# Optimization experiments

Measured on AMD Instinct MI355X. Metric: run time of the kernel, lower is better.

## Reference

```python
import jax, jax.numpy as jnp
import numpy as np

LN_EPS = 1e-5


def setup_inputs() -> dict:
    key = jax.random.key(0)
    ks = jax.random.split(key, 8)
    B, C, H, W = 16, 768, 64, 64
    cond_dim = 1024
    inp = {}
    inp["spatial_features"] = jax.random.normal(ks[0], (B, C, H, W), dtype=jnp.float32)
    inp["conditioning"] = jax.random.normal(ks[1], (B, cond_dim), dtype=jnp.float32)
    # conditioning_proj: Linear(cond_dim -> C)
    inp["w_cond"] = jax.random.normal(ks[2], (C, cond_dim), dtype=jnp.float32) * 0.02
    inp["b_cond"] = jnp.zeros((C,), dtype=jnp.float32)
    # MultiheadAttention packed in-projection [3C, C] and bias [3C]
    inp["in_proj_w"] = jax.random.normal(ks[3], (3 * C, C), dtype=jnp.float32) * 0.02
    inp["in_proj_b"] = jnp.zeros((3 * C,), dtype=jnp.float32)
    # MHA out_proj
    inp["attn_out_w"] = jax.random.normal(ks[4], (C, C), dtype=jnp.float32) * 0.02
    inp["attn_out_b"] = jnp.zeros((C,), dtype=jnp.float32)
    # output_proj Linear (dropout is identity at inference)
    inp["w_out"] = jax.random.normal(ks[5], (C, C), dtype=jnp.float32) * 0.02
    inp["b_out"] = jnp.zeros((C,), dtype=jnp.float32)
    # LayerNorm affine
    inp["ln_gamma"] = jnp.ones((C,), dtype=jnp.float32)
    inp["ln_beta"] = jnp.zeros((C,), dtype=jnp.float32)
    return inp


def reference(spatial_features, conditioning, w_cond, b_cond, in_proj_w, in_proj_b,
              attn_out_w, attn_out_b, w_out, b_out, ln_gamma, ln_beta):
    B, C, H, W = spatial_features.shape
    S = H * W
    # [B, C, H, W] -> [B, S, C]
    spatial_flat = spatial_features.reshape(B, C, S).transpose(0, 2, 1)
    # conditioning projection -> single KV token per batch: [B, C]
    cond = conditioning @ w_cond.T + b_cond
    # With a single key, softmax over the key axis is identically 1, so the
    # attention output is exactly the value vector broadcast over all queries;
    # Q and K projections have zero effect on output (and zero gradient).
    wv = in_proj_w[2 * C:]          # value rows of packed in-projection
    bv = in_proj_b[2 * C:]
    v = cond @ wv.T + bv            # [B, C]
    attn = v @ attn_out_w.T + attn_out_b  # MHA out_proj, [B, C]
    # output_proj (dropout = identity in eval)
    proj = attn @ w_out.T + b_out   # [B, C]
    # residual + LayerNorm over channel dim
    x = spatial_flat + proj[:, None, :]  # [B, S, C]
    mu = jnp.mean(x, axis=-1, keepdims=True)
    var = jnp.mean(jnp.square(x - mu), axis=-1, keepdims=True)
    y = (x - mu) * jax.lax.rsqrt(var + LN_EPS) * ln_gamma + ln_beta
    # [B, S, C] -> [B, C, H, W]
    return y.transpose(0, 2, 1).reshape(B, C, H, W)
```

## Files before the change

### kernel.cpp

```cpp
#include <hip/hip_runtime.h>

#define CDIM 768
#define SDIM 4096

typedef float nfloat4 __attribute__((ext_vector_type(4)));

__global__ __launch_bounds__(256) void small_gemm_kernel(
    const float* __restrict__ X, const float* __restrict__ W,
    const float* __restrict__ bias, float* __restrict__ out,
    int Cn, int K)
{
    int gid  = blockIdx.x * blockDim.x + threadIdx.x;
    int wid  = gid >> 6;
    int lane = threadIdx.x & 63;
    int total = 16 * Cn;
    if (wid >= total) return;
    int b = wid / Cn;
    int c = wid - b * Cn;
    const float* x = X + (size_t)b * K;
    const float* w = W + (size_t)c * K;
    float acc = 0.f;
    for (int k = lane * 4; k < K; k += 256) {
        float4 xv = *(const float4*)(x + k);
        float4 wv = *(const float4*)(w + k);
        acc += xv.x * wv.x + xv.y * wv.y + xv.z * wv.z + xv.w * wv.w;
    }
#pragma unroll
    for (int m = 32; m; m >>= 1) acc += __shfl_xor(acc, m, 64);
    if (lane == 0) out[wid] = acc + bias[c];
}

__global__ __launch_bounds__(256) void ln_stats(
    const float* __restrict__ sp, const float* __restrict__ proj,
    float* __restrict__ Aout, float* __restrict__ Bout)
{
    __shared__ float s_proj[CDIM];
    __shared__ float2 redA[4][64];
    __shared__ float2 redB[4][64];
    const int b  = blockIdx.y;
    const int s0 = blockIdx.x * 128;
    const int t  = threadIdx.x;
    for (int i = t; i < CDIM; i += 256) s_proj[i] = proj[b * CDIM + i];
    __syncthreads();

    const int lane = t & 63;
    const int wave = t >> 6;
    const float2* base = (const float2*)(sp + (size_t)b * CDIM * SDIM + s0) + lane;

    float2 A = make_float2(0.f, 0.f), B = make_float2(0.f, 0.f);
    const int cbeg = wave * (CDIM / 4);
    for (int c = cbeg; c < cbeg + CDIM / 4; c += 8) {
        float2 v[8];
#pragma unroll
        for (int k = 0; k < 8; ++k) v[k] = base[(size_t)(c + k) * (SDIM / 2)];
#pragma unroll
        for (int k = 0; k < 8; ++k) {
            float p  = s_proj[c + k];
            float ax = v[k].x + p, ay = v[k].y + p;
            A.x += ax;      A.y += ay;
            B.x += ax * ax; B.y += ay * ay;
        }
    }
    redA[wave][lane] = A;
    redB[wave][lane] = B;
    __syncthreads();

    if (t < 64) {
        float2 a = redA[0][t], bb = redB[0][t];
#pragma unroll
        for (int w = 1; w < 4; ++w) {
            a.x  += redA[w][t].x;  a.y  += redA[w][t].y;
            bb.x += redB[w][t].x;  bb.y += redB[w][t].y;
        }
        ((float2*)(Aout + (size_t)b * SDIM + s0))[t] = a;
        ((float2*)(Bout + (size_t)b * SDIM + s0))[t] = bb;
    }
}

__global__ __launch_bounds__(256) void ln_norm(
    const float* __restrict__ sp, const float* __restrict__ proj,
    const float* __restrict__ Ain, const float* __restrict__ Bin,
    const float* __restrict__ gamma, const float* __restrict__ beta,
    float* __restrict__ out)
{
    __shared__ float s_p[CDIM / 4], s_g[CDIM / 4], s_b[CDIM / 4];
    const int b      = blockIdx.y;
    const int s0     = blockIdx.x * 256;
    const int c_base = blockIdx.z * (CDIM / 4);
    const int t      = threadIdx.x;
    if (t < CDIM / 4) {
        s_p[t] = proj[b * CDIM + c_base + t];
        s_g[t] = gamma[c_base + t];
        s_b[t] = beta[c_base + t];
    }
    __syncthreads();

    const int lane = t & 63;
    const int wave = t >> 6;

    float4 A  = ((const float4*)(Ain + (size_t)b * SDIM + s0))[lane];
    float4 Bv = ((const float4*)(Bin + (size_t)b * SDIM + s0))[lane];
    const float inv = 1.f / CDIM;
    float4 mu, rs;
    mu.x = A.x * inv; mu.y = A.y * inv; mu.z = A.z * inv; mu.w = A.w * inv;
    rs.x = rsqrtf(Bv.x * inv - mu.x * mu.x + 1e-5f);
    rs.y = rsqrtf(Bv.y * inv - mu.y * mu.y + 1e-5f);
    rs.z = rsqrtf(Bv.z * inv - mu.z * mu.z + 1e-5f);
    rs.w = rsqrtf(Bv.w * inv - mu.w * mu.w + 1e-5f);

    const float4* spv  = (const float4*)(sp  + (size_t)b * CDIM * SDIM + s0) + lane;
    nfloat4*      outv = (nfloat4*)     (out + (size_t)b * CDIM * SDIM + s0) + lane;

    const int rbeg = wave * 48;
    for (int r = rbeg; r < rbeg + 48; r += 4) {
        float4 v[4];
#pragma unroll
        for (int k = 0; k < 4; ++k)
            v[k] = spv[(size_t)(c_base + r + k) * (SDIM / 4)];
#pragma unroll
        for (int k = 0; k < 4; ++k) {
            float p  = s_p[r + k];
            float g  = s_g[r + k];
            float be = s_b[r + k];
            nfloat4 y;
            y.x = (v[k].x + p - mu.x) * rs.x * g + be;
            y.y = (v[k].y + p - mu.y) * rs.y * g + be;
            y.z = (v[k].z + p - mu.z) * rs.z * g + be;
            y.w = (v[k].w + p - mu.w) * rs.w * g + be;
            __builtin_nontemporal_store(y, &outv[(size_t)(c_base + r + k) * (SDIM / 4)]);
        }
    }
}

extern "C" void kernel_launch(void* const* d_in, const int* in_sizes, int n_in,
                              void* d_out, int out_size, void* d_ws, size_t ws_size,
                              hipStream_t stream) {
    const float* sp           = (const float*)d_in[0];
    const float* conditioning = (const float*)d_in[1];
    const float* w_cond       = (const float*)d_in[2];
    const float* b_cond       = (const float*)d_in[3];
    const float* in_proj_w    = (const float*)d_in[4];
    const float* in_proj_b    = (const float*)d_in[5];
    const float* attn_out_w   = (const float*)d_in[6];
    const float* attn_out_b   = (const float*)d_in[7];
    const float* w_out        = (const float*)d_in[8];
    const float* b_out        = (const float*)d_in[9];
    const float* ln_gamma     = (const float*)d_in[10];
    const float* ln_beta      = (const float*)d_in[11];
    float* out = (float*)d_out;
    float* ws  = (float*)d_ws;

    float* cond = ws;
    float* v    = ws + 12288;
    float* attn = ws + 24576;
    float* proj = ws + 36864;
    float* Ast  = ws + 49152;
    float* Bst  = ws + 114688;

    const int gemm_blocks = (16 * CDIM) / 4;
    small_gemm_kernel<<<gemm_blocks, 256, 0, stream>>>(
        conditioning, w_cond, b_cond, cond, CDIM, 1024);
    small_gemm_kernel<<<gemm_blocks, 256, 0, stream>>>(
        cond, in_proj_w + 2 * CDIM * CDIM, in_proj_b + 2 * CDIM, v, CDIM, CDIM);
    small_gemm_kernel<<<gemm_blocks, 256, 0, stream>>>(
        v, attn_out_w, attn_out_b, attn, CDIM, CDIM);
    small_gemm_kernel<<<gemm_blocks, 256, 0, stream>>>(
        attn, w_out, b_out, proj, CDIM, CDIM);

    ln_stats<<<dim3(SDIM / 128, 16), 256, 0, stream>>>(sp, proj, Ast, Bst);
    ln_norm<<<dim3(SDIM / 256, 16, 4), 256, 0, stream>>>(
        sp, proj, Ast, Bst, ln_gamma, ln_beta, out);
}
```

Measured before the change: 411.0 us.

## Split LN stats over channel halves and narrow norm tiles for more blocks

The stats kernel now splits the channel reduction into two halves along a new grid z dimension, doubling block count. Partial sums are written interleaved as float4 (sum, sumsq pairs), and the norm kernel combines the two halves. The norm kernel switches from float4 to float2 accesses over 128-column tiles, doubling its grid and unrolling 8 rows per step. The aim is more parallelism and memory-level concurrency in the bandwidth-bound LayerNorm passes, at the cost of narrower vector loads and extra partial-stat traffic.

```diff
diff --git a/kernel.cpp b/kernel.cpp
--- a/kernel.cpp
+++ b/kernel.cpp
@@ -3,7 +3,7 @@
 #define CDIM 768
 #define SDIM 4096
 
-typedef float nfloat4 __attribute__((ext_vector_type(4)));
+typedef float nfloat2 __attribute__((ext_vector_type(2)));
 
 __global__ __launch_bounds__(256) void small_gemm_kernel(
     const float* __restrict__ X, const float* __restrict__ W,
@@ -32,30 +32,32 @@
 
 __global__ __launch_bounds__(256) void ln_stats(
     const float* __restrict__ sp, const float* __restrict__ proj,
-    float* __restrict__ Aout, float* __restrict__ Bout)
+    float4* __restrict__ AB)
 {
-    __shared__ float s_proj[CDIM];
+    __shared__ float s_proj[CDIM / 2];
     __shared__ float2 redA[4][64];
     __shared__ float2 redB[4][64];
     const int b  = blockIdx.y;
     const int s0 = blockIdx.x * 128;
+    const int z  = blockIdx.z;
     const int t  = threadIdx.x;
-    for (int i = t; i < CDIM; i += 256) s_proj[i] = proj[b * CDIM + i];
+    for (int i = t; i < CDIM / 2; i += 256) s_proj[i] = proj[b * CDIM + z * (CDIM / 2) + i];
     __syncthreads();
 
     const int lane = t & 63;
     const int wave = t >> 6;
-    const float2* base = (const float2*)(sp + (size_t)b * CDIM * SDIM + s0) + lane;
+    const float2* base = (const float2*)(sp + (size_t)b * CDIM * SDIM
+                                            + (size_t)z * (CDIM / 2) * SDIM + s0) + lane;
 
     float2 A = make_float2(0.f, 0.f), B = make_float2(0.f, 0.f);
-    const int cbeg = wave * (CDIM / 4);
-    for (int c = cbeg; c < cbeg + CDIM / 4; c += 8) {
+    const int lc0 = wave * 96;
+    for (int lc = lc0; lc < lc0 + 96; lc += 8) {
         float2 v[8];
 #pragma unroll
-        for (int k = 0; k < 8; ++k) v[k] = base[(size_t)(c + k) * (SDIM / 2)];
+        for (int k = 0; k < 8; ++k) v[k] = base[(size_t)(lc + k) * (SDIM / 2)];
 #pragma unroll
         for (int k = 0; k < 8; ++k) {
-            float p  = s_proj[c + k];
+            float p  = s_proj[lc + k];
             float ax = v[k].x + p, ay = v[k].y + p;
             A.x += ax;      A.y += ay;
             B.x += ax * ax; B.y += ay * ay;
@@ -72,20 +74,20 @@
             a.x  += redA[w][t].x;  a.y  += redA[w][t].y;
             bb.x += redB[w][t].x;  bb.y += redB[w][t].y;
         }
-        ((float2*)(Aout + (size_t)b * SDIM + s0))[t] = a;
-        ((float2*)(Bout + (size_t)b * SDIM + s0))[t] = bb;
+        AB[((size_t)z * 16 + b) * (SDIM / 2) + s0 / 2 + t] =
+            make_float4(a.x, bb.x, a.y, bb.y);
     }
 }
 
 __global__ __launch_bounds__(256) void ln_norm(
     const float* __restrict__ sp, const float* __restrict__ proj,
-    const float* __restrict__ Ain, const float* __restrict__ Bin,
+    const float4* __restrict__ AB,
     const float* __restrict__ gamma, const float* __restrict__ beta,
     float* __restrict__ out)
 {
     __shared__ float s_p[CDIM / 4], s_g[CDIM / 4], s_b[CDIM / 4];
     const int b      = blockIdx.y;
-    const int s0     = blockIdx.x * 256;
+    const int s0     = blockIdx.x * 128;
     const int c_base = blockIdx.z * (CDIM / 4);
     const int t      = threadIdx.x;
     if (t < CDIM / 4) {
@@ -98,36 +100,36 @@
     const int lane = t & 63;
     const int wave = t >> 6;
 
-    float4 A  = ((const float4*)(Ain + (size_t)b * SDIM + s0))[lane];
-    float4 Bv = ((const float4*)(Bin + (size_t)b * SDIM + s0))[lane];
+    float4 f0 = AB[((size_t)0 * 16 + b) * (SDIM / 2) + s0 / 2 + lane];
+    float4 f1 = AB[((size_t)1 * 16 + b) * (SDIM / 2) + s0 / 2 + lane];
     const float inv = 1.f / CDIM;
-    float4 mu, rs;
-    mu.x = A.x * inv; mu.y = A.y * inv; mu.z = A.z * inv; mu.w = A.w * inv;
-    rs.x = rsqrtf(Bv.x * inv - mu.x * mu.x + 1e-5f);
-    rs.y = rsqrtf(Bv.y * inv - mu.y * mu.y + 1e-5f);
-    rs.z = rsqrtf(Bv.z * inv - mu.z * mu.z + 1e-5f);
-    rs.w = rsqrtf(Bv.w * inv - mu.w * mu.w + 1e-5f);
+    float2 mu, rs;
+    mu.x = (f0.x + f1.x) * inv;
+    mu.y = (f0.z + f1.z) * inv;
+    rs.x = rsqrtf((f0.y + f1.y) * inv - mu.x * mu.x + 1e-5f);
+    rs.y = rsqrtf((f0.w + f1.w) * inv - mu.y * mu.y + 1e-5f);
 
-    const float4* spv  = (const float4*)(sp  + (size_t)b * CDIM * SDIM + s0) + lane;
-    nfloat4*      outv = (nfloat4*)     (out + (size_t)b * CDIM * SDIM + s0) + lane;
+    const float2* spv  = (const float2*)(sp  + (size_t)b * CDIM * SDIM
+                                             + (size_t)c_base * SDIM + s0) + lane;
+    nfloat2*      outv = (nfloat2*)     (out + (size_t)b * CDIM * SDIM
+                                             + (size_t)c_base * SDIM + s0) + lane;
 
     const int rbeg = wave * 48;
-    for (int r = rbeg; r < rbeg + 48; r += 4) {
-        float4 v[4];
+    for (int r = rbeg; r < rbeg + 48; r += 8) {
+        float2 v[8];
 #pragma unroll
-        for (int k = 0; k < 4; ++k)
-            v[k] = spv[(size_t)(c_base + r + k) * (SDIM / 4)];
+        for (int k = 0; k < 8; ++k)
+            v[k] = spv[(size_t)(r + k) * (SDIM / 2)];
 #pragma unroll
-        for (int k = 0; k < 4; ++k) {
+        for (int k = 0; k < 8; ++k) {
             float p  = s_p[r + k];
             float g  = s_g[r + k];
             float be = s_b[r + k];
-            nfloat4 y;
-            y.x = (v[k].x + p - mu.x) * rs.x * g + be;
-            y.y = (v[k].y + p - mu.y) * rs.y * g + be;
-            y.z = (v[k].z + p - mu.z) * rs.z * g + be;
-            y.w = (v[k].w + p - mu.w) * rs.w * g + be;
-            __builtin_nontemporal_store(y, &outv[(size_t)(c_base + r + k) * (SDIM / 4)]);
+            float gx = rs.x * g, gy = rs.y * g;
+            nfloat2 y;
+            y.x = (v[k].x + p - mu.x) * gx + be;
+            y.y = (v[k].y + p - mu.y) * gy + be;
+            __builtin_nontemporal_store(y, &outv[(size_t)(r + k) * (SDIM / 2)]);
         }
     }
 }
@@ -154,8 +156,7 @@
     float* v    = ws + 12288;
     float* attn = ws + 24576;
     float* proj = ws + 36864;
-    float* Ast  = ws + 49152;
-    float* Bst  = ws + 114688;
+    float4* AB  = (float4*)(ws + 49152);
 
     const int gemm_blocks = (16 * CDIM) / 4;
     small_gemm_kernel<<<gemm_blocks, 256, 0, stream>>>(
@@ -167,7 +168,7 @@
     small_gemm_kernel<<<gemm_blocks, 256, 0, stream>>>(
         attn, w_out, b_out, proj, CDIM, CDIM);
 
-    ln_stats<<<dim3(SDIM / 128, 16), 256, 0, stream>>>(sp, proj, Ast, Bst);
-    ln_norm<<<dim3(SDIM / 256, 16, 4), 256, 0, stream>>>(
-        sp, proj, Ast, Bst, ln_gamma, ln_beta, out);
+    ln_stats<<<dim3(SDIM / 128, 16, 2), 256, 0, stream>>>(sp, proj, AB);
+    ln_norm<<<dim3(SDIM / 128, 16, 4), 256, 0, stream>>>(
+        sp, proj, AB, ln_gamma, ln_beta, out);
 }
```

Result: no change. 410.1 us (-0.2%).
